# Kernel optimization log

Hardware: AMD Instinct MI355X
Metric: run time of the kernel (lower is better)

## Reference

```python
import jax, jax.numpy as jnp
import numpy as np

B, S, C, H = 1024, 254, 2, 1024
TIME_DIM = 64
HALF = TIME_DIM // 2
N_STEPS = 50


def time_embed(t):
    # t: [B] -> [B, 64] sinusoidal embedding, matching SinusoidalEmbedding(64)
    freqs = jnp.exp(jnp.arange(HALF, dtype=jnp.float32) * (-np.log(10000.0) / (HALF - 1)))
    ang = t[:, None] * freqs[None, :]  # [B, 32]
    return jnp.concatenate([jnp.sin(ang), jnp.cos(ang)], axis=-1)  # [B, 64]


def setup_inputs() -> dict:
    key = jax.random.key(0)
    ks = jax.random.split(key, 12)
    inp = {}
    inp["state"] = jax.random.normal(ks[0], (B, S), jnp.float32)
    inp["x0"] = jax.random.normal(ks[1], (B, C), jnp.float32)  # initial noise of sample()
    dims = [S + C + TIME_DIM, H, H, H, H, C]  # 320 -> 1024 x4 -> 2
    for i in range(5):
        kw, kb = jax.random.split(ks[2 + i])
        inp[f"W{i}"] = jax.random.normal(kw, (dims[i], dims[i + 1]), jnp.float32) * (1.0 / np.sqrt(dims[i]))
        inp[f"b{i}"] = jax.random.normal(kb, (dims[i + 1],), jnp.float32) * 0.01
    return inp


def reference(state, x0, W0, b0, W1, b1, W2, b2, W3, b3, W4, b4):
    dt = 1.0 / N_STEPS

    def velocity(x, t):
        temb = time_embed(t)
        h = jnp.concatenate([state, x, temb], axis=-1)  # [B, 320]
        h = jax.nn.silu(h @ W0 + b0)
        h = jax.nn.silu(h @ W1 + b1)
        h = jax.nn.silu(h @ W2 + b2)
        h = jax.nn.silu(h @ W3 + b3)
        return h @ W4 + b4  # [B, C]

    def step(x, i):
        t = jnp.full((state.shape[0],), i * dt, dtype=jnp.float32)
        return x + dt * velocity(x, t), None

    x, _ = jax.lax.scan(step, x0, jnp.arange(N_STEPS, dtype=jnp.float32))
    return x
```

## Files before the change

### kernel.cpp

```cpp
#include <hip/hip_runtime.h>


typedef __bf16 bf16x8 __attribute__((ext_vector_type(8)));
typedef float  f32x4  __attribute__((ext_vector_type(4)));
typedef float  f32x2  __attribute__((ext_vector_type(2)));
typedef unsigned short u16;
typedef u16 u16x8 __attribute__((ext_vector_type(8)));
typedef u16 u16x4 __attribute__((ext_vector_type(4)));
typedef u16 u16x2 __attribute__((ext_vector_type(2)));

#define H 1024
#define BATCH 1024
#define SDIM 254
#define NSTEP 50
#define DT 0.02f

__device__ __forceinline__ u16 f2bf(float f) {
  unsigned int u = __float_as_uint(f);
  return (u16)((u + 0x7FFFu + ((u >> 16) & 1u)) >> 16);
}

__device__ __forceinline__ float silu(float v) {
  return v / (1.0f + __expf(-v));
}

__global__ void transpose_w(const float* __restrict__ A, const float* __restrict__ B,
                            const float* __restrict__ C, u16* __restrict__ TA,
                            u16* __restrict__ TB, u16* __restrict__ TC) {
  const float* W = (blockIdx.z == 0) ? A : (blockIdx.z == 1) ? B : C;
  u16* T = (blockIdx.z == 0) ? TA : (blockIdx.z == 1) ? TB : TC;
  __shared__ float tile[32][33];
  const int n0 = blockIdx.x * 32, k0 = blockIdx.y * 32;
  const int tx = threadIdx.x & 31, ty = threadIdx.x >> 5;
#pragma unroll
  for (int i = 0; i < 4; ++i)
    tile[ty + 8 * i][tx] = W[(k0 + ty + 8 * i) * H + n0 + tx];
  __syncthreads();
#pragma unroll
  for (int i = 0; i < 4; ++i)
    T[(size_t)(n0 + ty + 8 * i) * H + k0 + tx] = f2bf(tile[tx][ty + 8 * i]);
}

__global__ __launch_bounds__(256) void base_gemm(const float* __restrict__ state,
                                                 const float* __restrict__ W0,
                                                 const float* __restrict__ b0,
                                                 u16* __restrict__ base16) {
  __shared__ float Sst[64][68];
  __shared__ float Wl[64][68];
  const int bc = blockIdx.x, br = blockIdx.y, tid = threadIdx.x;
  const int myrow = (tid >> 4) * 4;
  const int mycol = (tid & 15) * 4;
  const int lr = tid >> 2;
  const int lc = (tid & 3) * 16;
  f32x4 acc[4] = {};

  for (int kc = 0; kc < 4; ++kc) {
    const int k0 = kc * 64;
#pragma unroll
    for (int j = 0; j < 8; ++j) {
      const int k = k0 + lc + 2 * j;
      float vx = 0.f, vy = 0.f;
      if (k + 1 < SDIM) {
        float2 v = *(const float2*)&state[(size_t)(br * 64 + lr) * SDIM + k];
        vx = v.x; vy = v.y;
      } else if (k < SDIM) {
        vx = state[(size_t)(br * 64 + lr) * SDIM + k];
      }
      Sst[lr][lc + 2 * j] = vx;
      Sst[lr][lc + 2 * j + 1] = vy;
    }
#pragma unroll
    for (int j = 0; j < 4; ++j) {
      f32x4 wv = {};
      if (k0 + lr < SDIM)
        wv = *(const f32x4*)&W0[(size_t)(k0 + lr) * H + bc * 64 + lc + 4 * j];
      *(f32x4*)&Wl[lr][lc + 4 * j] = wv;
    }
    __syncthreads();
#pragma unroll 4
    for (int kk = 0; kk < 64; kk += 4) {
      f32x4 sv[4], wv[4];
#pragma unroll
      for (int r = 0; r < 4; ++r) sv[r] = *(const f32x4*)&Sst[myrow + r][kk];
#pragma unroll
      for (int j = 0; j < 4; ++j) wv[j] = *(const f32x4*)&Wl[kk + j][mycol];
#pragma unroll
      for (int r = 0; r < 4; ++r)
#pragma unroll
        for (int j = 0; j < 4; ++j)
          acc[r] += sv[r][j] * wv[j];
    }
    __syncthreads();
  }

  const f32x4 bv = *(const f32x4*)&b0[bc * 64 + mycol];
#pragma unroll
  for (int r = 0; r < 4; ++r) {
    u16x4 o;
#pragma unroll
    for (int e = 0; e < 4; ++e) o[e] = f2bf(acc[r][e] + bv[e]);
    *(u16x4*)&base16[(size_t)(br * 64 + myrow + r) * H + bc * 64 + mycol] = o;
  }
}

__global__ void tvec_kernel(const float* __restrict__ W0, u16* __restrict__ tvecb,
                            u16* __restrict__ wxa, u16* __restrict__ wxb) {
  const int s = blockIdx.x;
  const int h = blockIdx.y * 256 + threadIdx.x;
  if (s == NSTEP) {
    wxa[h] = f2bf(W0[254 * H + h]);
    wxb[h] = f2bf(W0[255 * H + h]);
    return;
  }
  const float t = (float)s * DT;
  float acc = 0.0f;
#pragma unroll
  for (int j = 0; j < 32; ++j) {
    float fr = __expf((float)j * (-9.210340371976184f / 31.0f));
    float ang = t * fr;
    acc += __sinf(ang) * W0[(256 + j) * H + h] + __cosf(ang) * W0[(288 + j) * H + h];
  }
  tvecb[s * H + h] = f2bf(acc);
}

__device__ __forceinline__ void mfma_all(const bf16x8 (&fa)[4][4],
                                         const bf16x8 (&fb)[4][4],
                                         f32x4 (&acc)[4][4]) {
#pragma unroll
  for (int it = 0; it < 4; ++it)
#pragma unroll
    for (int mt = 0; mt < 4; ++mt)
#pragma unroll
      for (int nt = 0; nt < 4; ++nt)
        acc[mt][nt] = __builtin_amdgcn_mfma_f32_16x16x32_bf16(fa[it][mt], fb[it][nt],
                                                              acc[mt][nt], 0, 0, 0);
}

__device__ __forceinline__ void load_frags(bf16x8 (&f)[4][4], const u16* __restrict__ P) {
#pragma unroll
  for (int it = 0; it < 4; ++it)
#pragma unroll
    for (int q = 0; q < 4; ++q)
      f[it][q] = *(const bf16x8*)(P + q * 16 * H + it * 32);
}

template <int TAIL>
__device__ __forceinline__ void reduce_epi(f32x4 (&acc)[4][4],
                                           const float* __restrict__ bias,
                                           u16* __restrict__ outp,
                                           const float* __restrict__ W4,
                                           float* __restrict__ vacc,
                                           int bn, int bm, int w, int lane, int tid,
                                           float (*red)[16][68]) {
  const int lr = lane & 15, quad = lane >> 4;
  const int m = tid >> 5, n0 = (tid & 31) * 2;
  const f32x2 bv = *(const f32x2*)&bias[bn * 64 + n0];
  f32x4 w4v = {};
  if (TAIL) w4v = *(const f32x4*)&W4[2 * (bn * 64 + n0)];
#pragma unroll
  for (int p = 0; p < 4; ++p) {
    if (p) __syncthreads();
#pragma unroll
    for (int nt = 0; nt < 4; ++nt)
#pragma unroll
      for (int r = 0; r < 4; ++r)
        red[w][quad * 4 + r][nt * 16 + lr] = acc[p][nt][r];
    __syncthreads();
    f32x2 sv = {};
#pragma unroll
    for (int ww = 0; ww < 8; ++ww) sv += *(const f32x2*)&red[ww][m][n0];
    const int gm = bm * 64 + p * 16 + m;
    if (!TAIL) {
      u16x2 o = {f2bf(silu(sv[0] + bv[0])), f2bf(silu(sv[1] + bv[1]))};
      *(u16x2*)&outp[(size_t)gm * H + bn * 64 + n0] = o;
    } else {
      const float t0 = silu(sv[0] + bv[0]), t1 = silu(sv[1] + bv[1]);
      float pv0 = t0 * w4v[0] + t1 * w4v[2];
      float pv1 = t0 * w4v[1] + t1 * w4v[3];
#pragma unroll
      for (int o = 16; o > 0; o >>= 1) {
        pv0 += __shfl_xor(pv0, o);
        pv1 += __shfl_xor(pv1, o);
      }
      if ((tid & 31) == 0) {
        atomicAdd(&vacc[2 * gm], pv0);
        atomicAdd(&vacc[2 * gm + 1], pv1);
      }
    }
  }
}

__global__ __launch_bounds__(512) void gemm_l1(
    const u16* __restrict__ base16, const u16* __restrict__ tvecb,
    const u16* __restrict__ wxa, const u16* __restrict__ wxb,
    const float* __restrict__ x0, const float* __restrict__ xrd,
    float* __restrict__ xwr, const float* __restrict__ vprev,
    const float* __restrict__ b4, const u16* __restrict__ w1t,
    const float* __restrict__ b1, u16* __restrict__ hB, int s) {
  __shared__ float red[8][16][68];
  __shared__ float2 xv[64];
  const int tid = threadIdx.x;
  const int w = tid >> 6, lane = tid & 63;
  const int lr = lane & 15, quad = lane >> 4;
  const int bn = blockIdx.x, bm = blockIdx.y;

  const u16* Bp = w1t + (size_t)(bn * 64 + lr) * H + w * 128 + quad * 8;
  bf16x8 fb[4][4];
  load_frags(fb, Bp);

  if (tid < 64) {
    const int gr = bm * 64 + tid;
    float2 xc;
    if (s == 0) {
      xc = *(const float2*)&x0[2 * gr];
    } else {
      float2 xp = *(const float2*)&xrd[2 * gr];
      xc.x = xp.x + DT * (vprev[2 * gr] + b4[0]);
      xc.y = xp.y + DT * (vprev[2 * gr + 1] + b4[1]);
    }
    xv[tid] = xc;
    if (bn == 0) *(float2*)&xwr[2 * gr] = xc;
  }
  __syncthreads();

  bf16x8 fa[4][4];
  const int kb = w * 128 + quad * 8;
#pragma unroll
  for (int it = 0; it < 4; ++it) {
    const int kq = kb + it * 32;
    const bf16x8 tv = *(const bf16x8*)&tvecb[(size_t)s * H + kq];
    const bf16x8 wa = *(const bf16x8*)&wxa[kq];
    const bf16x8 wb = *(const bf16x8*)&wxb[kq];
#pragma unroll
    for (int q = 0; q < 4; ++q) {
      const int r = lr + 16 * q;
      const bf16x8 bs = *(const bf16x8*)&base16[(size_t)(bm * 64 + r) * H + kq];
      const float2 xc = xv[r];
      u16x8 o;
#pragma unroll
      for (int e = 0; e < 8; ++e) {
        float v = (float)bs[e] + (float)tv[e] + xc.x * (float)wa[e] + xc.y * (float)wb[e];
        o[e] = f2bf(silu(v));
      }
      fa[it][q] = *(bf16x8*)&o;
    }
  }

  f32x4 acc[4][4] = {};
  mfma_all(fa, fb, acc);
  reduce_epi<0>(acc, b1, hB, nullptr, nullptr, bn, bm, w, lane, tid, red);
}

__global__ __launch_bounds__(512, 2) void gemm_l2(
    const u16* __restrict__ A, const u16* __restrict__ BT,
    const float* __restrict__ bias, u16* __restrict__ out,
    float* __restrict__ vzero) {
  __shared__ float red[8][16][68];
  const int tid = threadIdx.x;
  const int w = tid >> 6, lane = tid & 63;
  const int lr = lane & 15, quad = lane >> 4;
  const int bn = blockIdx.x, bm = blockIdx.y;

  if (bn == 0 && tid < 128) vzero[bm * 128 + tid] = 0.0f;

  const u16* Ap = A + (size_t)(bm * 64 + lr) * H + w * 128 + quad * 8;
  const u16* Bp = BT + (size_t)(bn * 64 + lr) * H + w * 128 + quad * 8;
  bf16x8 fa[4][4], fb[4][4];
  load_frags(fa, Ap);
  load_frags(fb, Bp);
  f32x4 acc[4][4] = {};
  mfma_all(fa, fb, acc);
  reduce_epi<0>(acc, bias, out, nullptr, nullptr, bn, bm, w, lane, tid, red);
}

__global__ __launch_bounds__(512, 2) void gemm_l3(
    const u16* __restrict__ A, const u16* __restrict__ BT,
    const float* __restrict__ b3, const float* __restrict__ W4,
    float* __restrict__ vacc) {
  __shared__ float red[8][16][68];
  const int tid = threadIdx.x;
  const int w = tid >> 6, lane = tid & 63;
  const int lr = lane & 15, quad = lane >> 4;
  const int bn = blockIdx.x, bm = blockIdx.y;

  const u16* Ap = A + (size_t)(bm * 64 + lr) * H + w * 128 + quad * 8;
  const u16* Bp = BT + (size_t)(bn * 64 + lr) * H + w * 128 + quad * 8;
  bf16x8 fa[4][4], fb[4][4];
  load_frags(fa, Ap);
  load_frags(fb, Bp);
  f32x4 acc[4][4] = {};
  mfma_all(fa, fb, acc);
  reduce_epi<1>(acc, b3, nullptr, W4, vacc, bn, bm, w, lane, tid, red);
}

__global__ void final_x(const float* __restrict__ xcur1, const float* __restrict__ vacc1,
                        const float* __restrict__ b4, float* __restrict__ xout) {
  const int i = blockIdx.x * 256 + threadIdx.x;
  xout[i] = xcur1[i] + DT * (vacc1[i] + b4[i & 1]);
}

extern "C" void kernel_launch(void* const* d_in, const int* in_sizes, int n_in,
                              void* d_out, int out_size, void* d_ws, size_t ws_size,
                              hipStream_t stream) {
  const float* state = (const float*)d_in[0];
  const float* x0    = (const float*)d_in[1];
  const float* W0    = (const float*)d_in[2];
  const float* b0    = (const float*)d_in[3];
  const float* W1    = (const float*)d_in[4];
  const float* b1    = (const float*)d_in[5];
  const float* W2    = (const float*)d_in[6];
  const float* b2    = (const float*)d_in[7];
  const float* W3    = (const float*)d_in[8];
  const float* b3    = (const float*)d_in[9];
  const float* W4    = (const float*)d_in[10];
  const float* b4    = (const float*)d_in[11];
  float* xout = (float*)d_out;

  char* ws = (char*)d_ws;
  const size_t MB = 1024 * 1024;
  const size_t KB = 1024;
  u16* base16 = (u16*)(ws + 0);
  u16* w1t = (u16*)(ws + 2 * MB);
  u16* w2t = (u16*)(ws + 4 * MB);
  u16* w3t = (u16*)(ws + 6 * MB);
  u16* hB  = (u16*)(ws + 8 * MB);
  u16* hC  = (u16*)(ws + 10 * MB);
  u16* tvecb = (u16*)(ws + 12 * MB);
  u16* wxa = (u16*)(ws + 12 * MB + 128 * KB);
  u16* wxb = (u16*)(ws + 12 * MB + 132 * KB);
  float* vacc = (float*)(ws + 12 * MB + 192 * KB);
  float* xcur = (float*)(ws + 12 * MB + 256 * KB);

  transpose_w<<<dim3(32, 32, 3), 256, 0, stream>>>(W1, W2, W3, w1t, w2t, w3t);
  base_gemm<<<dim3(16, 16), 256, 0, stream>>>(state, W0, b0, base16);
  tvec_kernel<<<dim3(NSTEP + 1, 4), 256, 0, stream>>>(W0, tvecb, wxa, wxb);

  for (int s = 0; s < NSTEP; ++s) {
    float* xrd = xcur + ((s + 1) & 1) * 2048;
    float* xwr = xcur + (s & 1) * 2048;
    float* vpr = vacc + ((s + 1) & 1) * 2048;
    float* vcu = vacc + (s & 1) * 2048;
    gemm_l1<<<dim3(16, 16), 512, 0, stream>>>(base16, tvecb, wxa, wxb, x0, xrd,
                                              xwr, vpr, b4, w1t, b1, hB, s);
    gemm_l2<<<dim3(16, 16), 512, 0, stream>>>(hB, w2t, b2, hC, vcu);
    gemm_l3<<<dim3(16, 16), 512, 0, stream>>>(hC, w3t, b3, W4, vcu);
  }
  final_x<<<dim3(8), 256, 0, stream>>>(xcur + 2048, vacc + 2048, b4, xout);
}
```

Before: 2.271 ms.

## Split layer-1 activation into tail kernel and use small-tile LDS MFMA GEMM

Moves the per-step x update and layer-0 activation (base + time + x terms, SiLU) out of the layer-1 GEMM into a separate tail kernel that writes a bf16 activation buffer. Layers 1 and 2 now use a new single-wavefront 32x32-tile GEMM that stages K-slices through LDS with register prefetch, replacing the 8-wave split-K kernel and its cross-wave LDS reduction. The tail kernel also zeroes the velocity accumulator and writes the final output, which removes final_x. The cost is one extra launch per step, and each small block keeps only one wave busy, so latency hiding is weaker.

```diff
diff --git a/kernel.cpp b/kernel.cpp
--- a/kernel.cpp
+++ b/kernel.cpp
@@ -14,10 +14,15 @@
 #define SDIM 254
 #define NSTEP 50
 #define DT 0.02f
+#define LDP 40
 
 __device__ __forceinline__ u16 f2bf(float f) {
   unsigned int u = __float_as_uint(f);
   return (u16)((u + 0x7FFFu + ((u >> 16) & 1u)) >> 16);
+}
+
+__device__ __forceinline__ float bf2f(u16 u) {
+  return __uint_as_float(((unsigned int)u) << 16);
 }
 
 __device__ __forceinline__ float silu(float v) {
@@ -123,6 +128,65 @@
   tvecb[s * H + h] = f2bf(acc);
 }
 
+__global__ __launch_bounds__(64) void gemm_mfma(const u16* __restrict__ A,
+                                                const u16* __restrict__ BT,
+                                                const float* __restrict__ bias,
+                                                u16* __restrict__ out) {
+  __shared__ u16 As[32 * LDP];
+  __shared__ u16 Bs[32 * LDP];
+  const int tid = threadIdx.x;
+  const int bn = blockIdx.x, bm = blockIdx.y;
+  const int lr = tid & 15, quad = tid >> 4;
+
+  const int srow = tid >> 2;
+  const int skc = (tid & 3) * 8;
+
+  const u16* Ap = A + (size_t)(bm * 32 + srow) * H + skc;
+  const u16* Bp = BT + (size_t)(bn * 32 + srow) * H + skc;
+
+  f32x4 acc[2][2] = {};
+
+  u16x8 ga0 = *(const u16x8*)(Ap);
+  u16x8 ga1 = *(const u16x8*)(Ap + 16 * H);
+  u16x8 gb0 = *(const u16x8*)(Bp);
+  u16x8 gb1 = *(const u16x8*)(Bp + 16 * H);
+
+  for (int kt = 0; kt < 32; ++kt) {
+    *(u16x8*)&As[srow * LDP + skc] = ga0;
+    *(u16x8*)&As[(srow + 16) * LDP + skc] = ga1;
+    *(u16x8*)&Bs[srow * LDP + skc] = gb0;
+    *(u16x8*)&Bs[(srow + 16) * LDP + skc] = gb1;
+    if (kt < 31) {
+      const int off = (kt + 1) * 32;
+      ga0 = *(const u16x8*)(Ap + off);
+      ga1 = *(const u16x8*)(Ap + 16 * H + off);
+      gb0 = *(const u16x8*)(Bp + off);
+      gb1 = *(const u16x8*)(Bp + 16 * H + off);
+    }
+    bf16x8 a0 = *(const bf16x8*)&As[lr * LDP + quad * 8];
+    bf16x8 a1 = *(const bf16x8*)&As[(16 + lr) * LDP + quad * 8];
+    bf16x8 b0 = *(const bf16x8*)&Bs[lr * LDP + quad * 8];
+    bf16x8 b1 = *(const bf16x8*)&Bs[(16 + lr) * LDP + quad * 8];
+    acc[0][0] = __builtin_amdgcn_mfma_f32_16x16x32_bf16(a0, b0, acc[0][0], 0, 0, 0);
+    acc[0][1] = __builtin_amdgcn_mfma_f32_16x16x32_bf16(a0, b1, acc[0][1], 0, 0, 0);
+    acc[1][0] = __builtin_amdgcn_mfma_f32_16x16x32_bf16(a1, b0, acc[1][0], 0, 0, 0);
+    acc[1][1] = __builtin_amdgcn_mfma_f32_16x16x32_bf16(a1, b1, acc[1][1], 0, 0, 0);
+  }
+
+#pragma unroll
+  for (int mt = 0; mt < 2; ++mt)
+#pragma unroll
+    for (int nt = 0; nt < 2; ++nt) {
+      const int gm = bm * 32 + mt * 16 + quad * 4;
+      const int gn = bn * 32 + nt * 16 + lr;
+      const float bv = bias[gn];
+      f32x4 v = acc[mt][nt];
+#pragma unroll
+      for (int r = 0; r < 4; ++r)
+        out[(size_t)(gm + r) * H + gn] = f2bf(silu(v[r] + bv));
+    }
+}
+
 __device__ __forceinline__ void mfma_all(const bf16x8 (&fa)[4][4],
                                          const bf16x8 (&fb)[4][4],
                                          f32x4 (&acc)[4][4]) {
@@ -142,135 +206,6 @@
 #pragma unroll
     for (int q = 0; q < 4; ++q)
       f[it][q] = *(const bf16x8*)(P + q * 16 * H + it * 32);
-}
-
-template <int TAIL>
-__device__ __forceinline__ void reduce_epi(f32x4 (&acc)[4][4],
-                                           const float* __restrict__ bias,
-                                           u16* __restrict__ outp,
-                                           const float* __restrict__ W4,
-                                           float* __restrict__ vacc,
-                                           int bn, int bm, int w, int lane, int tid,
-                                           float (*red)[16][68]) {
-  const int lr = lane & 15, quad = lane >> 4;
-  const int m = tid >> 5, n0 = (tid & 31) * 2;
-  const f32x2 bv = *(const f32x2*)&bias[bn * 64 + n0];
-  f32x4 w4v = {};
-  if (TAIL) w4v = *(const f32x4*)&W4[2 * (bn * 64 + n0)];
-#pragma unroll
-  for (int p = 0; p < 4; ++p) {
-    if (p) __syncthreads();
-#pragma unroll
-    for (int nt = 0; nt < 4; ++nt)
-#pragma unroll
-      for (int r = 0; r < 4; ++r)
-        red[w][quad * 4 + r][nt * 16 + lr] = acc[p][nt][r];
-    __syncthreads();
-    f32x2 sv = {};
-#pragma unroll
-    for (int ww = 0; ww < 8; ++ww) sv += *(const f32x2*)&red[ww][m][n0];
-    const int gm = bm * 64 + p * 16 + m;
-    if (!TAIL) {
-      u16x2 o = {f2bf(silu(sv[0] + bv[0])), f2bf(silu(sv[1] + bv[1]))};
-      *(u16x2*)&outp[(size_t)gm * H + bn * 64 + n0] = o;
-    } else {
-      const float t0 = silu(sv[0] + bv[0]), t1 = silu(sv[1] + bv[1]);
-      float pv0 = t0 * w4v[0] + t1 * w4v[2];
-      float pv1 = t0 * w4v[1] + t1 * w4v[3];
-#pragma unroll
-      for (int o = 16; o > 0; o >>= 1) {
-        pv0 += __shfl_xor(pv0, o);
-        pv1 += __shfl_xor(pv1, o);
-      }
-      if ((tid & 31) == 0) {
-        atomicAdd(&vacc[2 * gm], pv0);
-        atomicAdd(&vacc[2 * gm + 1], pv1);
-      }
-    }
-  }
-}
-
-__global__ __launch_bounds__(512) void gemm_l1(
-    const u16* __restrict__ base16, const u16* __restrict__ tvecb,
-    const u16* __restrict__ wxa, const u16* __restrict__ wxb,
-    const float* __restrict__ x0, const float* __restrict__ xrd,
-    float* __restrict__ xwr, const float* __restrict__ vprev,
-    const float* __restrict__ b4, const u16* __restrict__ w1t,
-    const float* __restrict__ b1, u16* __restrict__ hB, int s) {
-  __shared__ float red[8][16][68];
-  __shared__ float2 xv[64];
-  const int tid = threadIdx.x;
-  const int w = tid >> 6, lane = tid & 63;
-  const int lr = lane & 15, quad = lane >> 4;
-  const int bn = blockIdx.x, bm = blockIdx.y;
-
-  const u16* Bp = w1t + (size_t)(bn * 64 + lr) * H + w * 128 + quad * 8;
-  bf16x8 fb[4][4];
-  load_frags(fb, Bp);
-
-  if (tid < 64) {
-    const int gr = bm * 64 + tid;
-    float2 xc;
-    if (s == 0) {
-      xc = *(const float2*)&x0[2 * gr];
-    } else {
-      float2 xp = *(const float2*)&xrd[2 * gr];
-      xc.x = xp.x + DT * (vprev[2 * gr] + b4[0]);
-      xc.y = xp.y + DT * (vprev[2 * gr + 1] + b4[1]);
-    }
-    xv[tid] = xc;
-    if (bn == 0) *(float2*)&xwr[2 * gr] = xc;
-  }
-  __syncthreads();
-
-  bf16x8 fa[4][4];
-  const int kb = w * 128 + quad * 8;
-#pragma unroll
-  for (int it = 0; it < 4; ++it) {
-    const int kq = kb + it * 32;
-    const bf16x8 tv = *(const bf16x8*)&tvecb[(size_t)s * H + kq];
-    const bf16x8 wa = *(const bf16x8*)&wxa[kq];
-    const bf16x8 wb = *(const bf16x8*)&wxb[kq];
-#pragma unroll
-    for (int q = 0; q < 4; ++q) {
-      const int r = lr + 16 * q;
-      const bf16x8 bs = *(const bf16x8*)&base16[(size_t)(bm * 64 + r) * H + kq];
-      const float2 xc = xv[r];
-      u16x8 o;
-#pragma unroll
-      for (int e = 0; e < 8; ++e) {
-        float v = (float)bs[e] + (float)tv[e] + xc.x * (float)wa[e] + xc.y * (float)wb[e];
-        o[e] = f2bf(silu(v));
-      }
-      fa[it][q] = *(bf16x8*)&o;
-    }
-  }
-
-  f32x4 acc[4][4] = {};
-  mfma_all(fa, fb, acc);
-  reduce_epi<0>(acc, b1, hB, nullptr, nullptr, bn, bm, w, lane, tid, red);
-}
-
-__global__ __launch_bounds__(512, 2) void gemm_l2(
-    const u16* __restrict__ A, const u16* __restrict__ BT,
-    const float* __restrict__ bias, u16* __restrict__ out,
-    float* __restrict__ vzero) {
-  __shared__ float red[8][16][68];
-  const int tid = threadIdx.x;
-  const int w = tid >> 6, lane = tid & 63;
-  const int lr = lane & 15, quad = lane >> 4;
-  const int bn = blockIdx.x, bm = blockIdx.y;
-
-  if (bn == 0 && tid < 128) vzero[bm * 128 + tid] = 0.0f;
-
-  const u16* Ap = A + (size_t)(bm * 64 + lr) * H + w * 128 + quad * 8;
-  const u16* Bp = BT + (size_t)(bn * 64 + lr) * H + w * 128 + quad * 8;
-  bf16x8 fa[4][4], fb[4][4];
-  load_frags(fa, Ap);
-  load_frags(fb, Bp);
-  f32x4 acc[4][4] = {};
-  mfma_all(fa, fb, acc);
-  reduce_epi<0>(acc, bias, out, nullptr, nullptr, bn, bm, w, lane, tid, red);
 }
 
 __global__ __launch_bounds__(512, 2) void gemm_l3(
@@ -290,13 +225,80 @@
   load_frags(fb, Bp);
   f32x4 acc[4][4] = {};
   mfma_all(fa, fb, acc);
-  reduce_epi<1>(acc, b3, nullptr, W4, vacc, bn, bm, w, lane, tid, red);
-}
-
-__global__ void final_x(const float* __restrict__ xcur1, const float* __restrict__ vacc1,
-                        const float* __restrict__ b4, float* __restrict__ xout) {
-  const int i = blockIdx.x * 256 + threadIdx.x;
-  xout[i] = xcur1[i] + DT * (vacc1[i] + b4[i & 1]);
+
+  const int m = tid >> 5, n0 = (tid & 31) * 2;
+  const f32x2 bv = *(const f32x2*)&b3[bn * 64 + n0];
+  const f32x4 w4v = *(const f32x4*)&W4[2 * (bn * 64 + n0)];
+#pragma unroll
+  for (int p = 0; p < 4; ++p) {
+    if (p) __syncthreads();
+#pragma unroll
+    for (int nt = 0; nt < 4; ++nt)
+#pragma unroll
+      for (int r = 0; r < 4; ++r)
+        red[w][quad * 4 + r][nt * 16 + lr] = acc[p][nt][r];
+    __syncthreads();
+    f32x2 sv = {};
+#pragma unroll
+    for (int ww = 0; ww < 8; ++ww) sv += *(const f32x2*)&red[ww][m][n0];
+    const int gm = bm * 64 + p * 16 + m;
+    const float t0 = silu(sv[0] + bv[0]), t1 = silu(sv[1] + bv[1]);
+    float pv0 = t0 * w4v[0] + t1 * w4v[2];
+    float pv1 = t0 * w4v[1] + t1 * w4v[3];
+#pragma unroll
+    for (int o = 16; o > 0; o >>= 1) {
+      pv0 += __shfl_xor(pv0, o);
+      pv1 += __shfl_xor(pv1, o);
+    }
+    if ((tid & 31) == 0) {
+      atomicAdd(&vacc[2 * gm], pv0);
+      atomicAdd(&vacc[2 * gm + 1], pv1);
+    }
+  }
+}
+
+__global__ __launch_bounds__(256) void tail_kernel(
+    const u16* __restrict__ base16, const u16* __restrict__ tvecb,
+    const u16* __restrict__ wxa, const u16* __restrict__ wxb,
+    const float* __restrict__ x0, float* __restrict__ xcur,
+    float* __restrict__ vacc, const float* __restrict__ b4,
+    u16* __restrict__ hA, float* __restrict__ xout, int s) {
+  const int b = blockIdx.x, tid = threadIdx.x;
+  float2 xc;
+  if (s < 0) {
+    xc = *(const float2*)&x0[2 * b];
+  } else {
+    float2 xp = *(const float2*)&xcur[(size_t)(s & 1) * 2048 + 2 * b];
+    float2 vv = *(const float2*)&vacc[(size_t)(s & 1) * 2048 + 2 * b];
+    xc.x = xp.x + DT * (vv.x + b4[0]);
+    xc.y = xp.y + DT * (vv.y + b4[1]);
+  }
+  if (tid == 0) {
+    *(float2*)&xcur[(size_t)((s + 1) & 1) * 2048 + 2 * b] = xc;
+    float2 z = {0.f, 0.f};
+    if (s < 0) {
+      *(float2*)&vacc[2 * b] = z;
+      *(float2*)&vacc[2048 + 2 * b] = z;
+    } else {
+      *(float2*)&vacc[(size_t)((s + 1) & 1) * 2048 + 2 * b] = z;
+    }
+    if (s == NSTEP - 1) { xout[2 * b] = xc.x; xout[2 * b + 1] = xc.y; }
+  }
+  if (s < NSTEP - 1) {
+    const int n = tid * 4;
+    const int sp = s + 1;
+    const u16x4 bs = *(const u16x4*)&base16[(size_t)b * H + n];
+    const u16x4 tv = *(const u16x4*)&tvecb[(size_t)sp * H + n];
+    const u16x4 wa = *(const u16x4*)&wxa[n];
+    const u16x4 wb = *(const u16x4*)&wxb[n];
+    u16x4 o;
+#pragma unroll
+    for (int e = 0; e < 4; ++e) {
+      float v = bf2f(bs[e]) + bf2f(tv[e]) + xc.x * bf2f(wa[e]) + xc.y * bf2f(wb[e]);
+      o[e] = f2bf(silu(v));
+    }
+    *(u16x4*)&hA[(size_t)b * H + n] = o;
+  }
 }
 
 extern "C" void kernel_launch(void* const* d_in, const int* in_sizes, int n_in,
@@ -323,27 +325,26 @@
   u16* w1t = (u16*)(ws + 2 * MB);
   u16* w2t = (u16*)(ws + 4 * MB);
   u16* w3t = (u16*)(ws + 6 * MB);
-  u16* hB  = (u16*)(ws + 8 * MB);
-  u16* hC  = (u16*)(ws + 10 * MB);
-  u16* tvecb = (u16*)(ws + 12 * MB);
-  u16* wxa = (u16*)(ws + 12 * MB + 128 * KB);
-  u16* wxb = (u16*)(ws + 12 * MB + 132 * KB);
-  float* vacc = (float*)(ws + 12 * MB + 192 * KB);
-  float* xcur = (float*)(ws + 12 * MB + 256 * KB);
+  u16* hA  = (u16*)(ws + 8 * MB);
+  u16* hB  = (u16*)(ws + 10 * MB);
+  u16* hC  = (u16*)(ws + 12 * MB);
+  u16* tvecb = (u16*)(ws + 14 * MB);
+  u16* wxa = (u16*)(ws + 14 * MB + 128 * KB);
+  u16* wxb = (u16*)(ws + 14 * MB + 132 * KB);
+  float* vacc = (float*)(ws + 14 * MB + 192 * KB);
+  float* xcur = (float*)(ws + 14 * MB + 256 * KB);
 
   transpose_w<<<dim3(32, 32, 3), 256, 0, stream>>>(W1, W2, W3, w1t, w2t, w3t);
   base_gemm<<<dim3(16, 16), 256, 0, stream>>>(state, W0, b0, base16);
   tvec_kernel<<<dim3(NSTEP + 1, 4), 256, 0, stream>>>(W0, tvecb, wxa, wxb);
+  tail_kernel<<<BATCH, 256, 0, stream>>>(base16, tvecb, wxa, wxb, x0, xcur,
+                                         vacc, b4, hA, xout, -1);
 
   for (int s = 0; s < NSTEP; ++s) {
-    float* xrd = xcur + ((s + 1) & 1) * 2048;
-    float* xwr = xcur + (s & 1) * 2048;
-    float* vpr = vacc + ((s + 1) & 1) * 2048;
-    float* vcu = vacc + (s & 1) * 2048;
-    gemm_l1<<<dim3(16, 16), 512, 0, stream>>>(base16, tvecb, wxa, wxb, x0, xrd,
-                                              xwr, vpr, b4, w1t, b1, hB, s);
-    gemm_l2<<<dim3(16, 16), 512, 0, stream>>>(hB, w2t, b2, hC, vcu);
-    gemm_l3<<<dim3(16, 16), 512, 0, stream>>>(hC, w3t, b3, W4, vcu);
-  }
-  final_x<<<dim3(8), 256, 0, stream>>>(xcur + 2048, vacc + 2048, b4, xout);
-}
+    gemm_mfma<<<dim3(32, 32), 64, 0, stream>>>(hA, w1t, b1, hB);
+    gemm_mfma<<<dim3(32, 32), 64, 0, stream>>>(hB, w2t, b2, hC);
+    gemm_l3<<<dim3(16, 16), 512, 0, stream>>>(hC, w3t, b3, W4, vacc + (s & 1) * 2048);
+    tail_kernel<<<BATCH, 256, 0, stream>>>(base16, tvecb, wxa, wxb, x0, xcur,
+                                           vacc, b4, hA, xout, s);
+  }
+}
```

Result: faster. 1.860 ms (-18.1%).
